# Kernel optimization log

Hardware: AMD Instinct MI355X
Metric: run time of the kernel (lower is better)

The kernel has to match this reference:

```python
import jax, jax.numpy as jnp
import numpy as np
import math

D_MODEL = 1024
N_HEADS = 16
D_K = D_MODEL // N_HEADS
SEQ_LEN = 2048
BATCH = 2


def setup_inputs() -> dict:
    key = jax.random.key(0)
    ks = jax.random.split(key, 5)
    X = jax.random.normal(ks[0], (BATCH, SEQ_LEN, D_MODEL), dtype=jnp.float32)
    # Linear params (torch Linear: y = x @ W.T + b). Store as [in, out] for einsum.
    sc1 = 1.0 / math.sqrt(D_MODEL)
    W_qkv = jax.random.uniform(ks[1], (D_MODEL, 3 * D_MODEL), jnp.float32, -sc1, sc1)
    b_qkv = jax.random.uniform(ks[2], (3 * D_MODEL,), jnp.float32, -sc1, sc1)
    W_out = jax.random.uniform(ks[3], (D_MODEL, D_MODEL), jnp.float32, -sc1, sc1)
    b_out = jax.random.uniform(ks[4], (D_MODEL,), jnp.float32, -sc1, sc1)
    return {"X": X, "W_qkv": W_qkv, "b_qkv": b_qkv, "W_out": W_out, "b_out": b_out}


def reference(X, W_qkv, b_qkv, W_out, b_out):
    B, S, E = X.shape
    qkv = X @ W_qkv + b_qkv                       # [B,S,3E]
    qkv = qkv.reshape(B, S, 3, N_HEADS, D_K)
    q = jnp.transpose(qkv[:, :, 0], (0, 2, 1, 3))  # [B,H,S,Dk]
    k = jnp.transpose(qkv[:, :, 1], (0, 2, 1, 3))
    v = jnp.transpose(qkv[:, :, 2], (0, 2, 1, 3))
    scores = jnp.einsum('bhqd,bhkd->bhqk', q, k) / math.sqrt(D_K)
    causal = jnp.tril(jnp.ones((S, S), dtype=bool))
    scores = jnp.where(causal[None, None], scores, -jnp.inf)
    probs = jax.nn.softmax(scores, axis=-1)
    out = jnp.einsum('bhqk,bhkd->bhqd', probs, v)  # [B,H,S,Dk]
    out = jnp.transpose(out, (0, 2, 1, 3)).reshape(B, S, E)
    return out @ W_out + b_out
```

## Files before the change

kernel.cpp:

```cpp
#include <hip/hip_runtime.h>

typedef __bf16 bf16_t;
typedef bf16_t bf16x8 __attribute__((ext_vector_type(8)));
typedef bf16_t bf16x4 __attribute__((ext_vector_type(4)));
typedef float f32x4 __attribute__((ext_vector_type(4)));

#define SEQLEN 2048
#define EMB 1024
#define NHEADS 16
#define N3 3072
#define NBATCH 2
#define NEG_INF (-__builtin_inff())
#define SC2 0.18033688011112042f

__device__ __forceinline__ void async16(bf16_t* lds, const bf16_t* g) {
    __builtin_amdgcn_global_load_lds(
        (const __attribute__((address_space(1))) void*)g,
        (__attribute__((address_space(3))) void*)lds, 16, 0, 0);
}

__global__ __launch_bounds__(256) void transpose_w_bf16(
    const float* __restrict__ W, bf16_t* __restrict__ Wt, int K, int N,
    int scale_below)
{
    __shared__ float tile[64][65];
    const int n0 = blockIdx.x * 64, k0 = blockIdx.y * 64;
    const float s = (n0 < scale_below) ? SC2 : 1.0f;
    const int t = threadIdx.x;
    const int nl = t & 63, k4 = t >> 6;
#pragma unroll
    for (int i = 0; i < 16; ++i) {
        int kk = k4 + i * 4;
        tile[kk][nl] = W[(size_t)(k0 + kk) * N + n0 + nl];
    }
    __syncthreads();
    const int kl = t & 63, n4 = t >> 6;
#pragma unroll
    for (int i = 0; i < 16; ++i) {
        int nn = n4 + i * 4;
        Wt[(size_t)(n0 + nn) * K + k0 + kl] = (bf16_t)(tile[kl][nn] * s);
    }
}

__global__ __launch_bounds__(256) void scale_bias(
    const float* __restrict__ b, float* __restrict__ out)
{
    const int i = blockIdx.x * 256 + threadIdx.x;
    if (i < N3) out[i] = b[i] * (i < EMB ? SC2 : 1.0f);
}

__global__ __launch_bounds__(256) void cvt_f32_bf16(
    const float* __restrict__ in, bf16_t* __restrict__ out, int n)
{
    const int i = (blockIdx.x * 256 + threadIdx.x) * 8;
    if (i >= n) return;
    float4 a = *(const float4*)&in[i];
    float4 b = *(const float4*)&in[i + 4];
    bf16_t v[8];
    v[0] = (bf16_t)a.x; v[1] = (bf16_t)a.y; v[2] = (bf16_t)a.z; v[3] = (bf16_t)a.w;
    v[4] = (bf16_t)b.x; v[5] = (bf16_t)b.y; v[6] = (bf16_t)b.z; v[7] = (bf16_t)b.w;
    *(float4*)&out[i] = *(float4*)&v[0];
}

__global__ __launch_bounds__(256) void v_transpose(
    const bf16_t* __restrict__ qkv, bf16_t* __restrict__ vt)
{
    __shared__ bf16_t tile[64][72];
    const int bh = blockIdx.x & 31, st = blockIdx.x >> 5;
    const int b = bh >> 4, h = bh & 15;
    const int t = threadIdx.x;
    const int sr = t >> 2, dc = (t & 3) << 4;
    const bf16_t* src = &qkv[(size_t)(b * SEQLEN + st * 64 + sr) * N3 + 2 * EMB + h * 64 + dc];
    *(float4*)&tile[sr][dc]     = *(const float4*)src;
    *(float4*)&tile[sr][dc + 8] = *(const float4*)(src + 8);
    __syncthreads();
    const int d = t >> 2, scol = (t & 3) << 4;
    bf16_t v[16];
#pragma unroll
    for (int i = 0; i < 16; ++i) v[i] = tile[scol + i][d];
    bf16_t* dst = &vt[(size_t)(bh * 64 + d) * SEQLEN + st * 64 + scol];
    *(float4*)&dst[0] = *(float4*)&v[0];
    *(float4*)&dst[8] = *(float4*)&v[8];
}

template<bool OUT_BF16>
__global__ __launch_bounds__(256) void gemm_bt_kernel(
    const bf16_t* __restrict__ A, const bf16_t* __restrict__ Bt,
    const float* __restrict__ bias, void* __restrict__ Cp,
    int Mdim, int Ndim, int Kdim)
{
    __shared__ bf16_t As[128 * 32];
    __shared__ bf16_t Bs[128 * 32];
    const int nb = Ndim >> 7;
    const int cpx = gridDim.x >> 3;
    const int bid = (blockIdx.x & 7) * cpx + (blockIdx.x >> 3);
    const int bx = bid % nb, by = bid / nb;
    const int r0 = by << 7, c0 = bx << 7;
    const int t = threadIdx.x, lane = t & 63;
    const int wid = t >> 6;
    const int wm = wid >> 1, wn = wid & 1;
    const int lr = lane & 15, lg = lane >> 4;

    const int glrow = wid * 32 + (lane >> 2);
    const int glcol = (lane & 3) << 3;
    bf16_t* ldsA = &As[wid * 1024];
    bf16_t* ldsB = &Bs[wid * 1024];
    const bf16_t* gA = &A[(size_t)(r0 + glrow) * Kdim + glcol];
    const bf16_t* gB = &Bt[(size_t)(c0 + glrow) * Kdim + glcol];
    const size_t rowstep = (size_t)16 * Kdim;

    f32x4 acc[4][4] = {};
    const int KT = Kdim >> 5;
    for (int kt = 0; kt < KT; ++kt) {
        const int k0 = kt << 5;
        async16(ldsA,       gA + k0);
        async16(ldsA + 512, gA + k0 + rowstep);
        async16(ldsB,       gB + k0);
        async16(ldsB + 512, gB + k0 + rowstep);
        __syncthreads();
        bf16x8 af[4], bfm[4];
#pragma unroll
        for (int m = 0; m < 4; ++m)
            af[m] = *(const bf16x8*)&As[(wm * 64 + m * 16 + lr) * 32 + lg * 8];
#pragma unroll
        for (int n = 0; n < 4; ++n)
            bfm[n] = *(const bf16x8*)&Bs[(wn * 64 + n * 16 + lr) * 32 + lg * 8];
#pragma unroll
        for (int m = 0; m < 4; ++m)
#pragma unroll
            for (int n = 0; n < 4; ++n)
                acc[m][n] = __builtin_amdgcn_mfma_f32_16x16x32_bf16(
                    af[m], bfm[n], acc[m][n], 0, 0, 0);
        __syncthreads();
    }

#pragma unroll
    for (int m = 0; m < 4; ++m) {
#pragma unroll
        for (int n = 0; n < 4; ++n) {
            const int col = c0 + wn * 64 + n * 16 + lr;
            const float bval = bias[col];
#pragma unroll
            for (int j = 0; j < 4; ++j) {
                const int row = r0 + wm * 64 + m * 16 + lg * 4 + j;
                const float v = acc[m][n][j] + bval;
                if (OUT_BF16)
                    ((bf16_t*)Cp)[(size_t)row * Ndim + col] = (bf16_t)v;
                else
                    ((float*)Cp)[(size_t)row * Ndim + col] = v;
            }
        }
    }
}

__global__ __launch_bounds__(256, 4) void attn_kernel(
    const bf16_t* __restrict__ qkv, const bf16_t* __restrict__ vt,
    bf16_t* __restrict__ attn_out)
{
    __shared__ bf16_t Kl[2][4096];
    __shared__ bf16_t Vl[2][4096];
    const int d = blockIdx.x;
    const int r = d >> 8;
    const int u = (d >> 3) & 31;
    int qt = (r & 1) ? (31 - u) : u;
    if (r & 2) qt ^= 16;
    const int bh = (d & 7) + (r << 3);
    const int b = bh >> 4, h = bh & 15;
    const int q0 = qt << 6;
    const int t = threadIdx.x, lane = t & 63, wid = t >> 6;
    const int lr = lane & 15, lg = lane >> 4;
    const int sr = t >> 2, sc16 = (t & 3) << 4;

    const int fragb0 = (lr * 128 + lg * 16) ^ ((lr & 7) << 4);
    const int fragb1 = (lr * 128 + 64 + lg * 16) ^ ((lr & 7) << 4);
    const int stb0   = (sr * 128 + sc16 * 2) ^ ((sr & 7) << 4);
    const int stb1   = (sr * 128 + sc16 * 2 + 16) ^ ((sr & 7) << 4);

    const bf16_t* kp = &qkv[(size_t)(b * SEQLEN + sr) * N3 + EMB + h * 64 + sc16];
    const bf16_t* vp = &vt[(size_t)(bh * 64 + sr) * SEQLEN + sc16];
    const size_t kstep = (size_t)64 * N3;

    const int qg = q0 + wid * 16 + lr;
    bf16x8 qa0, qa1;
    {
        const bf16_t* qb = &qkv[(size_t)(b * SEQLEN + qg) * N3 + h * 64];
        qa0 = *(const bf16x8*)&qb[lg * 8];
        qa1 = *(const bf16x8*)&qb[32 + lg * 8];
    }
    f32x4 o[4] = {};
    float m_run = NEG_INF, l_run = 0.f;

    auto stK = [&](char* base, float4 a, float4 c) {
        *(float4*)(base + stb0) = a; *(float4*)(base + stb1) = c;
    };
    auto stV = [&](char* base, float4 a, float4 c) {
        float4 w0 = {a.x, a.y, c.x, c.y};
        float4 w1 = {a.z, a.w, c.z, c.w};
        *(float4*)(base + stb0) = w0; *(float4*)(base + stb1) = w1;
    };

    {
        float4 k0 = *(const float4*)kp, k1 = *(const float4*)(kp + 8);
        float4 v0 = *(const float4*)vp, v1 = *(const float4*)(vp + 8);
        stK((char*)Kl[0], k0, k1);
        stV((char*)Vl[0], v0, v1);
    }
    __syncthreads();
    int cur = 0;
    for (int kt = 0; kt <= qt; ++kt) {
        float4 nk0, nk1, nv0, nv1;
        const bool more = (kt < qt);
        if (more) {
            kp += kstep; vp += 64;
            nk0 = *(const float4*)kp; nk1 = *(const float4*)(kp + 8);
            nv0 = *(const float4*)vp; nv1 = *(const float4*)(vp + 8);
        }

        const char* Kc = (const char*)Kl[cur];
        const char* Vc = (const char*)Vl[cur];

        f32x4 sc[4] = {};
        __builtin_amdgcn_s_setprio(1);
#pragma unroll
        for (int n = 0; n < 4; ++n) {
            bf16x8 kb0 = *(const bf16x8*)(Kc + (fragb0 + n * 2048));
            bf16x8 kb1 = *(const bf16x8*)(Kc + (fragb1 + n * 2048));
            sc[n] = __builtin_amdgcn_mfma_f32_16x16x32_bf16(kb0, qa0, sc[n], 0, 0, 0);
            sc[n] = __builtin_amdgcn_mfma_f32_16x16x32_bf16(kb1, qa1, sc[n], 0, 0, 0);
        }
        __builtin_amdgcn_s_setprio(0);

        if (kt == qt) {
#pragma unroll
            for (int n = 0; n < 4; ++n)
#pragma unroll
                for (int j = 0; j < 4; ++j) {
                    const int kg = kt * 64 + n * 16 + lg * 4 + j;
                    sc[n][j] = (kg <= qg) ? sc[n][j] : NEG_INF;
                }
        }
        float mx[4];
#pragma unroll
        for (int n = 0; n < 4; ++n)
            mx[n] = fmaxf(fmaxf(fmaxf(sc[n][0], sc[n][1]), sc[n][2]), sc[n][3]);
        float pmax = fmaxf(fmaxf(fmaxf(mx[0], mx[1]), mx[2]), mx[3]);

        if (__any(pmax > m_run + 8.f)) {
            float pm = fmaxf(pmax, __shfl_xor(pmax, 16));
            pm = fmaxf(pm, __shfl_xor(pm, 32));
            const float mnew = fmaxf(m_run, pm);
            const float alpha = exp2f(m_run - mnew);
            m_run = mnew;
            l_run *= alpha;
            float al[4];
#pragma unroll
            for (int j = 0; j < 4; ++j) al[j] = __shfl(alpha, lg * 4 + j);
#pragma unroll
            for (int dn = 0; dn < 4; ++dn)
#pragma unroll
                for (int j = 0; j < 4; ++j) o[dn][j] *= al[j];
        }

        float rs[4];
#pragma unroll
        for (int n = 0; n < 4; ++n) {
#pragma unroll
            for (int j = 0; j < 4; ++j) sc[n][j] = exp2f(sc[n][j] - m_run);
            rs[n] = (sc[n][0] + sc[n][1]) + (sc[n][2] + sc[n][3]);
        }
        l_run += (rs[0] + rs[1]) + (rs[2] + rs[3]);

        unsigned pk00, pk01, pk10, pk11, pk20, pk21, pk30, pk31;
        asm("v_cvt_pk_bf16_f32 %0, %1, %2" : "=v"(pk00) : "v"(sc[0][0]), "v"(sc[0][1]));
        asm("v_cvt_pk_bf16_f32 %0, %1, %2" : "=v"(pk01) : "v"(sc[0][2]), "v"(sc[0][3]));
        asm("v_cvt_pk_bf16_f32 %0, %1, %2" : "=v"(pk10) : "v"(sc[1][0]), "v"(sc[1][1]));
        asm("v_cvt_pk_bf16_f32 %0, %1, %2" : "=v"(pk11) : "v"(sc[1][2]), "v"(sc[1][3]));
        asm("v_cvt_pk_bf16_f32 %0, %1, %2" : "=v"(pk20) : "v"(sc[2][0]), "v"(sc[2][1]));
        asm("v_cvt_pk_bf16_f32 %0, %1, %2" : "=v"(pk21) : "v"(sc[2][2]), "v"(sc[2][3]));
        asm("v_cvt_pk_bf16_f32 %0, %1, %2" : "=v"(pk30) : "v"(sc[3][0]), "v"(sc[3][1]));
        asm("v_cvt_pk_bf16_f32 %0, %1, %2" : "=v"(pk31) : "v"(sc[3][2]), "v"(sc[3][3]));
        asm("v_permlane32_swap_b32 %0, %1" : "+v"(pk00), "+v"(pk10));
        asm("v_permlane32_swap_b32 %0, %1" : "+v"(pk01), "+v"(pk11));
        asm("v_permlane32_swap_b32 %0, %1" : "+v"(pk20), "+v"(pk30));
        asm("v_permlane32_swap_b32 %0, %1" : "+v"(pk21), "+v"(pk31));
        union UW { unsigned w[4]; bf16x8 v; };
        UW ua, ub;
        ua.w[0] = pk00; ua.w[1] = pk01; ua.w[2] = pk10; ua.w[3] = pk11;
        ub.w[0] = pk20; ub.w[1] = pk21; ub.w[2] = pk30; ub.w[3] = pk31;
        const bf16x8 pa0 = ua.v, pa1 = ub.v;

        __builtin_amdgcn_s_setprio(1);
#pragma unroll
        for (int dn = 0; dn < 4; ++dn) {
            bf16x8 vb0 = *(const bf16x8*)(Vc + (fragb0 + dn * 2048));
            bf16x8 vb1 = *(const bf16x8*)(Vc + (fragb1 + dn * 2048));
            o[dn] = __builtin_amdgcn_mfma_f32_16x16x32_bf16(pa0, vb0, o[dn], 0, 0, 0);
            o[dn] = __builtin_amdgcn_mfma_f32_16x16x32_bf16(pa1, vb1, o[dn], 0, 0, 0);
        }
        __builtin_amdgcn_s_setprio(0);

        if (more) {
            stK((char*)Kl[cur ^ 1], nk0, nk1);
            stV((char*)Vl[cur ^ 1], nv0, nv1);
        }
        __syncthreads();
        cur ^= 1;
    }

    float lt = l_run;
    lt += __shfl_xor(lt, 16);
    lt += __shfl_xor(lt, 32);
    float li[4];
#pragma unroll
    for (int j = 0; j < 4; ++j) li[j] = 1.0f / __shfl(lt, lg * 4 + j);
#pragma unroll
    for (int dn = 0; dn < 4; ++dn)
#pragma unroll
        for (int j = 0; j < 4; ++j) {
            const int row = b * SEQLEN + q0 + wid * 16 + lg * 4 + j;
            attn_out[(size_t)row * EMB + h * 64 + dn * 16 + lr] =
                (bf16_t)(o[dn][j] * li[j]);
        }
}

extern "C" void kernel_launch(void* const* d_in, const int* in_sizes, int n_in,
                              void* d_out, int out_size, void* d_ws, size_t ws_size,
                              hipStream_t stream)
{
    const float* X     = (const float*)d_in[0];
    const float* W_qkv = (const float*)d_in[1];
    const float* b_qkv = (const float*)d_in[2];
    const float* W_out = (const float*)d_in[3];
    const float* b_out = (const float*)d_in[4];
    float* out = (float*)d_out;

    char* ws = (char*)d_ws;
    bf16_t* Wqkv_t = (bf16_t*)ws;
    bf16_t* Wout_t = (bf16_t*)(ws + 6u * 1024 * 1024);
    bf16_t* qkv    = (bf16_t*)(ws + 8u * 1024 * 1024);
    bf16_t* attn   = (bf16_t*)(ws + 32u * 1024 * 1024);
    bf16_t* Xb     = (bf16_t*)(ws + 40u * 1024 * 1024);
    bf16_t* Vt_g   = (bf16_t*)(ws + 48u * 1024 * 1024);
    float*  bq_s   = (float*)(ws + 56u * 1024 * 1024);

    dim3 blk(256);
    transpose_w_bf16<<<dim3(N3 / 64, EMB / 64), blk, 0, stream>>>(W_qkv, Wqkv_t, EMB, N3, EMB);
    transpose_w_bf16<<<dim3(EMB / 64, EMB / 64), blk, 0, stream>>>(W_out, Wout_t, EMB, EMB, 0);
    scale_bias<<<(N3 + 255) / 256, blk, 0, stream>>>(b_qkv, bq_s);
    cvt_f32_bf16<<<4096 * 1024 / (256 * 8), blk, 0, stream>>>(X, Xb, 4096 * 1024);

    gemm_bt_kernel<true><<<(4096 / 128) * (N3 / 128), blk, 0, stream>>>(
        Xb, Wqkv_t, bq_s, (void*)qkv, 4096, N3, EMB);

    v_transpose<<<32 * (SEQLEN / 64), blk, 0, stream>>>(qkv, Vt_g);

    attn_kernel<<<32 * 32, blk, 0, stream>>>(qkv, Vt_g, attn);

    gemm_bt_kernel<false><<<(4096 / 128) * (EMB / 128), blk, 0, stream>>>(
        attn, Wout_t, b_out, (void*)out, 4096, EMB, EMB);
}
```

Baseline: 128.6 us.

## Fuse V transpose and bias scaling into QKV GEMM, compute row sums via MFMA

Merges the two weight-transpose launches into one kernel and folds the q-bias scaling into the GEMM epilogue, which removes the scale_bias kernel. The QKV GEMM epilogue now writes V tiles directly in transposed layout, so the separate v_transpose pass and its extra read/write of V are gone. In attention, the softmax row sum is accumulated with an extra MFMA against a ones vector, replacing the per-lane adds and the final cross-lane shuffles. This cuts three launches and some VALU work, at the cost of narrow 8-byte strided stores in the GEMM epilogue and two extra MFMAs per tile.

```diff
diff --git a/kernel.cpp b/kernel.cpp
--- a/kernel.cpp
+++ b/kernel.cpp
@@ -19,13 +19,17 @@
         (__attribute__((address_space(3))) void*)lds, 16, 0, 0);
 }
 
-__global__ __launch_bounds__(256) void transpose_w_bf16(
-    const float* __restrict__ W, bf16_t* __restrict__ Wt, int K, int N,
-    int scale_below)
+__global__ __launch_bounds__(256) void transpose_weights(
+    const float* __restrict__ Wqkv, const float* __restrict__ Wout,
+    bf16_t* __restrict__ Wqkv_t, bf16_t* __restrict__ Wout_t)
 {
     __shared__ float tile[64][65];
-    const int n0 = blockIdx.x * 64, k0 = blockIdx.y * 64;
-    const float s = (n0 < scale_below) ? SC2 : 1.0f;
+    int bx = blockIdx.x;
+    const int k0 = blockIdx.y * 64;
+    const float* W; bf16_t* Wt; int N; float s;
+    if (bx < 48) { W = Wqkv; Wt = Wqkv_t; N = N3;  s = (bx * 64 < EMB) ? SC2 : 1.0f; }
+    else         { bx -= 48; W = Wout; Wt = Wout_t; N = EMB; s = 1.0f; }
+    const int n0 = bx * 64;
     const int t = threadIdx.x;
     const int nl = t & 63, k4 = t >> 6;
 #pragma unroll
@@ -38,15 +42,8 @@
 #pragma unroll
     for (int i = 0; i < 16; ++i) {
         int nn = n4 + i * 4;
-        Wt[(size_t)(n0 + nn) * K + k0 + kl] = (bf16_t)(tile[kl][nn] * s);
-    }
-}
-
-__global__ __launch_bounds__(256) void scale_bias(
-    const float* __restrict__ b, float* __restrict__ out)
-{
-    const int i = blockIdx.x * 256 + threadIdx.x;
-    if (i < N3) out[i] = b[i] * (i < EMB ? SC2 : 1.0f);
+        Wt[(size_t)(n0 + nn) * EMB + k0 + kl] = (bf16_t)(tile[kl][nn] * s);
+    }
 }
 
 __global__ __launch_bounds__(256) void cvt_f32_bf16(
@@ -62,31 +59,11 @@
     *(float4*)&out[i] = *(float4*)&v[0];
 }
 
-__global__ __launch_bounds__(256) void v_transpose(
-    const bf16_t* __restrict__ qkv, bf16_t* __restrict__ vt)
-{
-    __shared__ bf16_t tile[64][72];
-    const int bh = blockIdx.x & 31, st = blockIdx.x >> 5;
-    const int b = bh >> 4, h = bh & 15;
-    const int t = threadIdx.x;
-    const int sr = t >> 2, dc = (t & 3) << 4;
-    const bf16_t* src = &qkv[(size_t)(b * SEQLEN + st * 64 + sr) * N3 + 2 * EMB + h * 64 + dc];
-    *(float4*)&tile[sr][dc]     = *(const float4*)src;
-    *(float4*)&tile[sr][dc + 8] = *(const float4*)(src + 8);
-    __syncthreads();
-    const int d = t >> 2, scol = (t & 3) << 4;
-    bf16_t v[16];
-#pragma unroll
-    for (int i = 0; i < 16; ++i) v[i] = tile[scol + i][d];
-    bf16_t* dst = &vt[(size_t)(bh * 64 + d) * SEQLEN + st * 64 + scol];
-    *(float4*)&dst[0] = *(float4*)&v[0];
-    *(float4*)&dst[8] = *(float4*)&v[8];
-}
-
-template<bool OUT_BF16>
+template<bool OUT_BF16, bool V_SPLIT>
 __global__ __launch_bounds__(256) void gemm_bt_kernel(
     const bf16_t* __restrict__ A, const bf16_t* __restrict__ Bt,
     const float* __restrict__ bias, void* __restrict__ Cp,
+    bf16_t* __restrict__ vt, int scale_q,
     int Mdim, int Ndim, int Kdim)
 {
     __shared__ bf16_t As[128 * 32];
@@ -134,20 +111,32 @@
         __syncthreads();
     }
 
+    const bool vmode = V_SPLIT && (c0 >= 2 * EMB);
 #pragma unroll
     for (int m = 0; m < 4; ++m) {
 #pragma unroll
         for (int n = 0; n < 4; ++n) {
             const int col = c0 + wn * 64 + n * 16 + lr;
-            const float bval = bias[col];
-#pragma unroll
-            for (int j = 0; j < 4; ++j) {
-                const int row = r0 + wm * 64 + m * 16 + lg * 4 + j;
-                const float v = acc[m][n][j] + bval;
-                if (OUT_BF16)
-                    ((bf16_t*)Cp)[(size_t)row * Ndim + col] = (bf16_t)v;
-                else
-                    ((float*)Cp)[(size_t)row * Ndim + col] = v;
+            float bval = bias[col];
+            if (scale_q && col < EMB) bval *= SC2;
+            if (vmode) {
+                const int h = (col - 2 * EMB) >> 6, dd = col & 63;
+                const int bb = r0 >> 11;
+                const int sbase = (r0 & (SEQLEN - 1)) + wm * 64 + m * 16 + lg * 4;
+                bf16x4 pk;
+#pragma unroll
+                for (int j = 0; j < 4; ++j) pk[j] = (bf16_t)(acc[m][n][j] + bval);
+                *(bf16x4*)&vt[(size_t)((bb * 16 + h) * 64 + dd) * SEQLEN + sbase] = pk;
+            } else {
+#pragma unroll
+                for (int j = 0; j < 4; ++j) {
+                    const int row = r0 + wm * 64 + m * 16 + lg * 4 + j;
+                    const float v = acc[m][n][j] + bval;
+                    if (OUT_BF16)
+                        ((bf16_t*)Cp)[(size_t)row * Ndim + col] = (bf16_t)v;
+                    else
+                        ((float*)Cp)[(size_t)row * Ndim + col] = v;
+                }
             }
         }
     }
@@ -187,8 +176,13 @@
         qa0 = *(const bf16x8*)&qb[lg * 8];
         qa1 = *(const bf16x8*)&qb[32 + lg * 8];
     }
+    bf16x8 ones;
+#pragma unroll
+    for (int i = 0; i < 8; ++i) ones[i] = (bf16_t)1.0f;
+
     f32x4 o[4] = {};
-    float m_run = NEG_INF, l_run = 0.f;
+    f32x4 ol = {};
+    float m_run = NEG_INF;
 
     auto stK = [&](char* base, float4 a, float4 c) {
         *(float4*)(base + stb0) = a; *(float4*)(base + stb1) = c;
@@ -251,7 +245,6 @@
             const float mnew = fmaxf(m_run, pm);
             const float alpha = exp2f(m_run - mnew);
             m_run = mnew;
-            l_run *= alpha;
             float al[4];
 #pragma unroll
             for (int j = 0; j < 4; ++j) al[j] = __shfl(alpha, lg * 4 + j);
@@ -259,16 +252,14 @@
             for (int dn = 0; dn < 4; ++dn)
 #pragma unroll
                 for (int j = 0; j < 4; ++j) o[dn][j] *= al[j];
-        }
-
-        float rs[4];
-#pragma unroll
-        for (int n = 0; n < 4; ++n) {
+#pragma unroll
+            for (int j = 0; j < 4; ++j) ol[j] *= al[j];
+        }
+
+#pragma unroll
+        for (int n = 0; n < 4; ++n)
 #pragma unroll
             for (int j = 0; j < 4; ++j) sc[n][j] = exp2f(sc[n][j] - m_run);
-            rs[n] = (sc[n][0] + sc[n][1]) + (sc[n][2] + sc[n][3]);
-        }
-        l_run += (rs[0] + rs[1]) + (rs[2] + rs[3]);
 
         unsigned pk00, pk01, pk10, pk11, pk20, pk21, pk30, pk31;
         asm("v_cvt_pk_bf16_f32 %0, %1, %2" : "=v"(pk00) : "v"(sc[0][0]), "v"(sc[0][1]));
@@ -297,6 +288,8 @@
             o[dn] = __builtin_amdgcn_mfma_f32_16x16x32_bf16(pa0, vb0, o[dn], 0, 0, 0);
             o[dn] = __builtin_amdgcn_mfma_f32_16x16x32_bf16(pa1, vb1, o[dn], 0, 0, 0);
         }
+        ol = __builtin_amdgcn_mfma_f32_16x16x32_bf16(pa0, ones, ol, 0, 0, 0);
+        ol = __builtin_amdgcn_mfma_f32_16x16x32_bf16(pa1, ones, ol, 0, 0, 0);
         __builtin_amdgcn_s_setprio(0);
 
         if (more) {
@@ -307,12 +300,9 @@
         cur ^= 1;
     }
 
-    float lt = l_run;
-    lt += __shfl_xor(lt, 16);
-    lt += __shfl_xor(lt, 32);
     float li[4];
 #pragma unroll
-    for (int j = 0; j < 4; ++j) li[j] = 1.0f / __shfl(lt, lg * 4 + j);
+    for (int j = 0; j < 4; ++j) li[j] = 1.0f / ol[j];
 #pragma unroll
     for (int dn = 0; dn < 4; ++dn)
 #pragma unroll
@@ -341,21 +331,16 @@
     bf16_t* attn   = (bf16_t*)(ws + 32u * 1024 * 1024);
     bf16_t* Xb     = (bf16_t*)(ws + 40u * 1024 * 1024);
     bf16_t* Vt_g   = (bf16_t*)(ws + 48u * 1024 * 1024);
-    float*  bq_s   = (float*)(ws + 56u * 1024 * 1024);
 
     dim3 blk(256);
-    transpose_w_bf16<<<dim3(N3 / 64, EMB / 64), blk, 0, stream>>>(W_qkv, Wqkv_t, EMB, N3, EMB);
-    transpose_w_bf16<<<dim3(EMB / 64, EMB / 64), blk, 0, stream>>>(W_out, Wout_t, EMB, EMB, 0);
-    scale_bias<<<(N3 + 255) / 256, blk, 0, stream>>>(b_qkv, bq_s);
+    transpose_weights<<<dim3(64, 16), blk, 0, stream>>>(W_qkv, W_out, Wqkv_t, Wout_t);
     cvt_f32_bf16<<<4096 * 1024 / (256 * 8), blk, 0, stream>>>(X, Xb, 4096 * 1024);
 
-    gemm_bt_kernel<true><<<(4096 / 128) * (N3 / 128), blk, 0, stream>>>(
-        Xb, Wqkv_t, bq_s, (void*)qkv, 4096, N3, EMB);
-
-    v_transpose<<<32 * (SEQLEN / 64), blk, 0, stream>>>(qkv, Vt_g);
+    gemm_bt_kernel<true, true><<<(4096 / 128) * (N3 / 128), blk, 0, stream>>>(
+        Xb, Wqkv_t, b_qkv, (void*)qkv, Vt_g, 1, 4096, N3, EMB);
 
     attn_kernel<<<32 * 32, blk, 0, stream>>>(qkv, Vt_g, attn);
 
-    gemm_bt_kernel<false><<<(4096 / 128) * (EMB / 128), blk, 0, stream>>>(
-        attn, Wout_t, b_out, (void*)out, 4096, EMB, EMB);
-}
+    gemm_bt_kernel<false, false><<<(4096 / 128) * (EMB / 128), blk, 0, stream>>>(
+        attn, Wout_t, b_out, (void*)out, nullptr, 0, 4096, EMB, EMB);
+}
```

New measurement: 119.0 us. -7.4%, faster.
